# Kernel optimization log

Measured on AMD Instinct MI355X. Metric: run time of the kernel, lower is better.

Reference implementation:

```python
import jax, jax.numpy as jnp
import numpy as np

H = 12
D_MODEL = 768
D_K = D_MODEL // H  # 64


def setup_inputs() -> dict:
    key = jax.random.key(0)
    ks = jax.random.split(key, 16)
    B, S, D = 4, 1024, D_MODEL
    scale = 1.0 / np.sqrt(D)
    inp = {
        "query": jax.random.normal(ks[0], (B, S, D), jnp.float32),
        "key": jax.random.normal(ks[1], (B, S, D), jnp.float32),
        "value": jax.random.normal(ks[2], (B, S, D), jnp.float32),
        "times": jax.random.normal(ks[3], (2, B, S, D), jnp.float32),
        # learned params (Linear weights stored torch-style [out, in])
        "Wq": jax.random.normal(ks[4], (D, D), jnp.float32) * scale,
        "bq": jnp.zeros((D,), jnp.float32),
        "Wk": jax.random.normal(ks[5], (D, D), jnp.float32) * scale,
        "bk": jnp.zeros((D,), jnp.float32),
        "Wv": jax.random.normal(ks[6], (D, D), jnp.float32) * scale,
        "bv": jnp.zeros((D,), jnp.float32),
        "Wt": jax.random.normal(ks[7], (D, D), jnp.float32) * scale,
        "bt": jnp.zeros((D,), jnp.float32),
        "Wo": jax.random.normal(ks[8], (D, D), jnp.float32) * scale,
        "bo": jnp.zeros((D,), jnp.float32),
    }
    return inp


def _split_heads(x, B, S):
    # [B,S,D] -> [B,H,S,D_K]
    return x.reshape(B, S, H, D_K).transpose(0, 2, 1, 3)


def reference(query, key, value, times, Wq, bq, Wk, bk, Wv, bv, Wt, bt, Wo, bo):
    B, S, D = query.shape
    inv_sqrt_dk = 1.0 / jnp.sqrt(jnp.asarray(D_K, query.dtype))
    # q/k/v projections are identical across time-loop iterations; hoist them.
    q = _split_heads(query @ Wq.T + bq, B, S)   # [B,H,S,dk]
    k = _split_heads(key @ Wk.T + bk, B, S)
    v = _split_heads(value @ Wv.T + bv, B, S)
    x = jnp.zeros_like(q)
    n_times = times.shape[0]
    for i in range(n_times):  # small fixed loop over time embeddings
        t = _split_heads(times[i] @ Wt.T + bt, B, S)
        # dual-score attention: query.time + query.key, each scaled by 1/sqrt(d_k)
        scores = (jnp.einsum('bhqd,bhkd->bhqk', q, t)
                  + jnp.einsum('bhqd,bhkd->bhqk', q, k)) * inv_sqrt_dk
        p = jax.nn.softmax(scores, axis=-1)
        x = x + jnp.einsum('bhqk,bhkd->bhqd', p, v)
    x = x.transpose(0, 2, 1, 3).reshape(B, S, H * D_K)
    return x @ Wo.T + bo
```

## Files before the change

kernel.cpp:

```cpp
#include <hip/hip_runtime.h>
#include <hip/hip_fp16.h>

typedef _Float16 v8h __attribute__((ext_vector_type(8)));
typedef _Float16 v4h __attribute__((ext_vector_type(4)));
typedef float v4f __attribute__((ext_vector_type(4)));

#define MFMA_F16 __builtin_amdgcn_mfma_f32_16x16x32_f16
#define MFMA16_F16 __builtin_amdgcn_mfma_f32_16x16x16f16
#define EXP2F __builtin_amdgcn_exp2f

__device__ static inline void async_copy16(const void* g, void* l) {
  __builtin_amdgcn_global_load_lds(
      (const __attribute__((address_space(1))) void*)g,
      (__attribute__((address_space(3))) void*)l, 16, 0, 0);
}

struct CastArgs {
  const float* src[10];
  _Float16* dst[10];
  int n8[10];
  float scale[10];
};
__global__ void cast_all(CastArgs a) {
  const int z = blockIdx.y;
  const int i = blockIdx.x * 256 + threadIdx.x;
  if (i >= a.n8[z]) return;
  const float sc = a.scale[z];
  const float* s = a.src[z] + (size_t)i * 8;
  const float4 f0 = *(const float4*)s;
  const float4 f1 = *(const float4*)(s + 4);
  v8h o = {(_Float16)(f0.x * sc), (_Float16)(f0.y * sc),
           (_Float16)(f0.z * sc), (_Float16)(f0.w * sc),
           (_Float16)(f1.x * sc), (_Float16)(f1.y * sc),
           (_Float16)(f1.z * sc), (_Float16)(f1.w * sc)};
  *(v8h*)(a.dst[z] + (size_t)i * 8) = o;
}

struct GemmArgs {
  const _Float16* A1[4]; const _Float16* A2[4];
  const _Float16* W1[4]; const _Float16* W2[4];
  const float* b1[4];    const float* b2[4];
  void* out[4];
  float bscale[4];
  int K[4];
  int mode[4];
};

__global__ __launch_bounds__(256) void gemm_mt(GemmArgs g) {
  __shared__ _Float16 a_lds[128 * 64];
  __shared__ _Float16 w_lds[128 * 64];
  const int z = blockIdx.z;
  const int KK = g.K[z];
  const int tid = threadIdx.x;
  const int w = tid >> 6, lane = tid & 63, quad = lane >> 4, l16 = lane & 15;
  const int m0 = blockIdx.x * 128, n0 = blockIdx.y * 128;
  const int wm = (w >> 1) * 64, wn = (w & 1) * 64;

  size_t srcOff[4]; int ldsOff[4];
  #pragma unroll
  for (int i = 0; i < 4; ++i) {
    const int c = i * 256 + tid, row = c >> 3, slot = c & 7;
    srcOff[i] = (size_t)row * 768 + (size_t)((slot ^ (row & 7)) * 8);
    ldsOff[i] = (i * 256 + w * 64) * 8;
  }

  v4f acc[4][4] = {};

  for (int k0 = 0; k0 < KK; k0 += 64) {
    const _Float16* Asrc = (k0 < 768) ? g.A1[z] : g.A2[z];
    const _Float16* Wsrc = (k0 < 768) ? g.W1[z] : g.W2[z];
    const int kc = (k0 < 768) ? k0 : k0 - 768;
    __syncthreads();
    #pragma unroll
    for (int i = 0; i < 4; ++i) {
      async_copy16(Asrc + (size_t)m0 * 768 + kc + srcOff[i], &a_lds[ldsOff[i]]);
      async_copy16(Wsrc + (size_t)n0 * 768 + kc + srcOff[i], &w_lds[ldsOff[i]]);
    }
    __syncthreads();

    #pragma unroll
    for (int kh = 0; kh < 2; ++kh) {
      v8h af[4], bf[4];
      #pragma unroll
      for (int mt = 0; mt < 4; ++mt) {
        const int r = wm + mt * 16 + l16;
        af[mt] = *(const v8h*)&a_lds[r * 64 + (((kh * 4 + quad) ^ (r & 7)) * 8)];
      }
      #pragma unroll
      for (int nt = 0; nt < 4; ++nt) {
        const int r = wn + nt * 16 + l16;
        bf[nt] = *(const v8h*)&w_lds[r * 64 + (((kh * 4 + quad) ^ (r & 7)) * 8)];
      }
      #pragma unroll
      for (int mt = 0; mt < 4; ++mt)
        #pragma unroll
        for (int nt = 0; nt < 4; ++nt)
          acc[mt][nt] = MFMA_F16(af[mt], bf[nt], acc[mt][nt], 0, 0, 0);
    }
  }

  const int mode = g.mode[z];
  #pragma unroll
  for (int nt = 0; nt < 4; ++nt) {
    const int col = n0 + wn + nt * 16 + l16;
    float bv = g.b1[z][col] * g.bscale[z];
    if (g.b2[z]) bv += g.b2[z][col];
    if (mode == 1) {
      _Float16* outp = (_Float16*)g.out[z];
      const int h = col >> 6, dk = col & 63;
      #pragma unroll
      for (int mt = 0; mt < 4; ++mt) {
        const int row = m0 + wm + mt * 16 + quad * 4;
        const int b = row >> 10, s = row & 1023;
        const int sp = (s & ~31) | ((s & 12) << 1) | ((s & 16) >> 2);
        v4h pack = {(_Float16)(acc[mt][nt][0] + bv), (_Float16)(acc[mt][nt][1] + bv),
                    (_Float16)(acc[mt][nt][2] + bv), (_Float16)(acc[mt][nt][3] + bv)};
        *(v4h*)&outp[(size_t)((b * 12 + h) * 64 + dk) * 1024 + sp] = pack;
      }
    } else {
      #pragma unroll
      for (int mt = 0; mt < 4; ++mt)
        #pragma unroll
        for (int r = 0; r < 4; ++r) {
          const int row = m0 + wm + mt * 16 + quad * 4 + r;
          const float v = acc[mt][nt][r] + bv;
          if (mode == 2) ((float*)g.out[z])[(size_t)row * 768 + col] = v;
          else ((_Float16*)g.out[z])[(size_t)row * 768 + col] = (_Float16)v;
        }
    }
  }
}

__global__ __launch_bounds__(256) void attn(
    const _Float16* __restrict__ Q,
    const _Float16* __restrict__ KT0, const _Float16* __restrict__ KT1,
    const _Float16* __restrict__ Vt,
    _Float16* __restrict__ X)
{
  __shared__ _Float16 kt0[2][64 * 64];
  __shared__ _Float16 kt1[2][64 * 64];
  __shared__ _Float16 vt[2][64 * 64];

  const int tid = threadIdx.x;
  const int w = tid >> 6, lane = tid & 63, quad = lane >> 4, l16 = lane & 15;
  const int bh = blockIdx.y, b = bh / 12, h = bh % 12;
  const int q0 = blockIdx.x * 64;
  const size_t base = (size_t)b * 1024 * 768 + h * 64;

  const _Float16* KT0b = KT0 + base;
  const _Float16* KT1b = KT1 + base;
  const _Float16* Vtb = Vt + (size_t)bh * 64 * 1024;

  size_t ktOff[2], vOff[2]; int ldsOff[2];
  #pragma unroll
  for (int i = 0; i < 2; ++i) {
    const int c = i * 256 + w * 64 + lane, row = c >> 3, slot = c & 7;
    const int logical = slot ^ (row & 7);
    ktOff[i] = (size_t)row * 768 + (size_t)(logical * 8);
    vOff[i] = (size_t)row * 1024 + (size_t)(logical * 8);
    ldsOff[i] = c * 8;
  }
  auto stage = [&](int kv0, int buf) {
    #pragma unroll
    for (int i = 0; i < 2; ++i) {
      async_copy16(KT0b + (size_t)kv0 * 768 + ktOff[i], &kt0[buf][ldsOff[i]]);
      async_copy16(KT1b + (size_t)kv0 * 768 + ktOff[i], &kt1[buf][ldsOff[i]]);
      async_copy16(Vtb + (size_t)kv0 + vOff[i], &vt[buf][ldsOff[i]]);
    }
  };

  const _Float16* Qw = Q + base + (size_t)(q0 + w * 16) * 768;
  const v8h qf0 = *(const v8h*)(Qw + (size_t)l16 * 768 + quad * 8);
  const v8h qf1 = *(const v8h*)(Qw + (size_t)l16 * 768 + 32 + quad * 8);

  const v4h ones = {(_Float16)1.f, (_Float16)1.f, (_Float16)1.f, (_Float16)1.f};
  v4f o[2][4] = {};
  v4f osum[2] = {};

  stage(0, 0);
  for (int cc = 0; cc < 16; ++cc) {
    __syncthreads();
    if (cc < 15) stage((cc + 1) * 64, (cc + 1) & 1);
    const _Float16* k0p = &kt0[cc & 1][0];
    const _Float16* k1p = &kt1[cc & 1][0];
    const _Float16* vp = &vt[cc & 1][0];

    v4f s[2][4];
    #pragma unroll
    for (int kvt = 0; kvt < 4; ++kvt) {
      const int r = kvt * 16 + l16, rw = r & 7;
      const v8h k00 = *(const v8h*)&k0p[r * 64 + ((quad ^ rw) * 8)];
      const v8h k01 = *(const v8h*)&k0p[r * 64 + (((4 + quad) ^ rw) * 8)];
      const v8h k10 = *(const v8h*)&k1p[r * 64 + ((quad ^ rw) * 8)];
      const v8h k11 = *(const v8h*)&k1p[r * 64 + (((4 + quad) ^ rw) * 8)];
      s[0][kvt] = MFMA_F16(k00, qf0, v4f{}, 0, 0, 0);
      s[0][kvt] = MFMA_F16(k01, qf1, s[0][kvt], 0, 0, 0);
      s[1][kvt] = MFMA_F16(k10, qf0, v4f{}, 0, 0, 0);
      s[1][kvt] = MFMA_F16(k11, qf1, s[1][kvt], 0, 0, 0);
    }

    v4h pb[2][4];
    #pragma unroll
    for (int t = 0; t < 2; ++t)
      #pragma unroll
      for (int kvt = 0; kvt < 4; ++kvt) {
        pb[t][kvt] = v4h{(_Float16)EXP2F(s[t][kvt][0]),
                         (_Float16)EXP2F(s[t][kvt][1]),
                         (_Float16)EXP2F(s[t][kvt][2]),
                         (_Float16)EXP2F(s[t][kvt][3])};
        osum[t] = MFMA16_F16(ones, pb[t][kvt], osum[t], 0, 0, 0);
      }

    #pragma unroll
    for (int dkt = 0; dkt < 4; ++dkt) {
      const int row = dkt * 16 + l16, rw = row & 7;
      #pragma unroll
      for (int gph = 0; gph < 2; ++gph) {
        const int phys = (gph * 4 + quad) ^ rw;
        const v8h vv = *(const v8h*)&vp[row * 64 + phys * 8];
        const v4h lo = {vv[0], vv[1], vv[2], vv[3]};
        const v4h hi = {vv[4], vv[5], vv[6], vv[7]};
        #pragma unroll
        for (int t = 0; t < 2; ++t) {
          o[t][dkt] = MFMA16_F16(lo, pb[t][gph * 2], o[t][dkt], 0, 0, 0);
          o[t][dkt] = MFMA16_F16(hi, pb[t][gph * 2 + 1], o[t][dkt], 0, 0, 0);
        }
      }
    }
  }

  const float i0 = 1.0f / osum[0][0], i1 = 1.0f / osum[1][0];

  _Float16* Xw = X + base + (size_t)(q0 + w * 16 + l16) * 768;
  #pragma unroll
  for (int dkt = 0; dkt < 4; ++dkt) {
    v4h pack;
    #pragma unroll
    for (int r = 0; r < 4; ++r)
      pack[r] = (_Float16)(o[0][dkt][r] * i0 + o[1][dkt][r] * i1);
    *(v4h*)&Xw[dkt * 16 + quad * 4] = pack;
  }
}

extern "C" void kernel_launch(void* const* d_in, const int* in_sizes, int n_in,
                              void* d_out, int out_size, void* d_ws, size_t ws_size,
                              hipStream_t stream) {
  const float* query = (const float*)d_in[0];
  const float* key   = (const float*)d_in[1];
  const float* value = (const float*)d_in[2];
  const float* times = (const float*)d_in[3];
  const float* Wq = (const float*)d_in[4];  const float* bq = (const float*)d_in[5];
  const float* Wk = (const float*)d_in[6];  const float* bk = (const float*)d_in[7];
  const float* Wv = (const float*)d_in[8];  const float* bv = (const float*)d_in[9];
  const float* Wt = (const float*)d_in[10]; const float* bt = (const float*)d_in[11];
  const float* Wo = (const float*)d_in[12]; const float* bo = (const float*)d_in[13];
  float* out = (float*)d_out;

  const size_t NELEM = (size_t)4096 * 768;
  const size_t WELEM = (size_t)768 * 768;
  const float QSCALE = 0.125f * 1.4426950408889634f;

  char* ws = (char*)d_ws;
  size_t off = 0;
  auto alloc = [&](size_t bytes) {
    void* p = ws + off; off += (bytes + 255) & ~(size_t)255; return p;
  };
  _Float16* qh  = (_Float16*)alloc(NELEM * 2);
  _Float16* kh  = (_Float16*)alloc(NELEM * 2);
  _Float16* vh  = (_Float16*)alloc(NELEM * 2);
  _Float16* wqh = (_Float16*)alloc(WELEM * 2);
  _Float16* wkh = (_Float16*)alloc(WELEM * 2);
  _Float16* wvh = (_Float16*)alloc(WELEM * 2);
  _Float16* wth = (_Float16*)alloc(WELEM * 2);
  _Float16* woh = (_Float16*)alloc(WELEM * 2);
  _Float16* Qh  = (_Float16*)alloc(NELEM * 2);
  _Float16* KT0 = (_Float16*)alloc(NELEM * 2);
  _Float16* KT1 = (_Float16*)alloc(NELEM * 2);
  _Float16* Vt  = (_Float16*)alloc(NELEM * 2);
  _Float16* t0h = (_Float16*)d_out;
  _Float16* t1h = t0h + NELEM;
  _Float16* Xh = qh;

  CastArgs ca = {};
  const int nA8 = (int)(NELEM / 8), nW8 = (int)(WELEM / 8);
  const float* csrc[10] = {query, key, value, times, times + NELEM, Wq, Wk, Wv, Wt, Wo};
  _Float16* cdst[10] = {qh, kh, vh, t0h, t1h, wqh, wkh, wvh, wth, woh};
  for (int i = 0; i < 10; ++i) {
    ca.src[i] = csrc[i]; ca.dst[i] = cdst[i];
    ca.n8[i] = (i < 5) ? nA8 : nW8;
    ca.scale[i] = (i == 5) ? QSCALE : 1.0f;
  }
  cast_all<<<dim3((nA8 + 255) / 256, 10), 256, 0, stream>>>(ca);

  GemmArgs pa = {};
  pa.A1[0] = t0h; pa.A2[0] = kh; pa.W1[0] = wth; pa.W2[0] = wkh;
  pa.b1[0] = bt; pa.b2[0] = bk; pa.out[0] = KT0; pa.bscale[0] = 1.0f;
  pa.K[0] = 1536; pa.mode[0] = 0;
  pa.A1[1] = t1h; pa.A2[1] = kh; pa.W1[1] = wth; pa.W2[1] = wkh;
  pa.b1[1] = bt; pa.b2[1] = bk; pa.out[1] = KT1; pa.bscale[1] = 1.0f;
  pa.K[1] = 1536; pa.mode[1] = 0;
  pa.A1[2] = qh; pa.A2[2] = qh; pa.W1[2] = wqh; pa.W2[2] = wqh;
  pa.b1[2] = bq; pa.b2[2] = nullptr; pa.out[2] = Qh; pa.bscale[2] = QSCALE;
  pa.K[2] = 768; pa.mode[2] = 0;
  pa.A1[3] = vh; pa.A2[3] = vh; pa.W1[3] = wvh; pa.W2[3] = wvh;
  pa.b1[3] = bv; pa.b2[3] = nullptr; pa.out[3] = Vt; pa.bscale[3] = 1.0f;
  pa.K[3] = 768; pa.mode[3] = 1;
  gemm_mt<<<dim3(32, 6, 4), 256, 0, stream>>>(pa);

  attn<<<dim3(16, 48), 256, 0, stream>>>(Qh, KT0, KT1, Vt, Xh);

  GemmArgs oa = {};
  oa.A1[0] = Xh; oa.A2[0] = Xh; oa.W1[0] = woh; oa.W2[0] = woh;
  oa.b1[0] = bo; oa.b2[0] = nullptr; oa.out[0] = out; oa.bscale[0] = 1.0f;
  oa.K[0] = 768; oa.mode[0] = 2;
  gemm_mt<<<dim3(32, 6, 1), 256, 0, stream>>>(oa);
}
```

Baseline: 237.8 us.

## Use 16x16x32 MFMA for PV, flatten cast grid, smaller output-GEMM tiles

The attention PV and row-sum products switch from the 16x16x16 MFMA to the 16x16x32 MFMA. P is packed with cvt_pkrtz into 8-wide fp16 vectors so each V LDS read feeds a single MFMA. The main loop is unrolled by two so LDS buffer pointers become constants. The cast kernel moves from a 2D grid with idle blocks for the small weight tensors to a flat 1D grid with prefix offsets. The output projection GEMM uses a templated 64-row tile so it launches twice as many blocks. These changes cut instruction count, wasted blocks and output-GEMM underfill, at the cost of round-toward-zero fp16 conversion of the probabilities.

```diff
diff --git a/kernel.cpp b/kernel.cpp
--- a/kernel.cpp
+++ b/kernel.cpp
@@ -3,11 +3,15 @@
 
 typedef _Float16 v8h __attribute__((ext_vector_type(8)));
 typedef _Float16 v4h __attribute__((ext_vector_type(4)));
+typedef _Float16 v2h __attribute__((ext_vector_type(2)));
 typedef float v4f __attribute__((ext_vector_type(4)));
 
 #define MFMA_F16 __builtin_amdgcn_mfma_f32_16x16x32_f16
-#define MFMA16_F16 __builtin_amdgcn_mfma_f32_16x16x16f16
 #define EXP2F __builtin_amdgcn_exp2f
+
+__device__ static inline v2h pkrtz(float a, float b) {
+  return __builtin_bit_cast(v2h, __builtin_amdgcn_cvt_pkrtz(a, b));
+}
 
 __device__ static inline void async_copy16(const void* g, void* l) {
   __builtin_amdgcn_global_load_lds(
@@ -18,22 +22,25 @@
 struct CastArgs {
   const float* src[10];
   _Float16* dst[10];
-  int n8[10];
+  int start[11];
   float scale[10];
 };
 __global__ void cast_all(CastArgs a) {
-  const int z = blockIdx.y;
-  const int i = blockIdx.x * 256 + threadIdx.x;
-  if (i >= a.n8[z]) return;
+  const int g = blockIdx.x * 256 + threadIdx.x;
+  if (g >= a.start[10]) return;
+  int z = 0;
+  #pragma unroll
+  for (int i = 1; i < 10; ++i) if (g >= a.start[i]) z = i;
+  const int i0 = g - a.start[z];
   const float sc = a.scale[z];
-  const float* s = a.src[z] + (size_t)i * 8;
+  const float* s = a.src[z] + (size_t)i0 * 8;
   const float4 f0 = *(const float4*)s;
   const float4 f1 = *(const float4*)(s + 4);
   v8h o = {(_Float16)(f0.x * sc), (_Float16)(f0.y * sc),
            (_Float16)(f0.z * sc), (_Float16)(f0.w * sc),
            (_Float16)(f1.x * sc), (_Float16)(f1.y * sc),
            (_Float16)(f1.z * sc), (_Float16)(f1.w * sc)};
-  *(v8h*)(a.dst[z] + (size_t)i * 8) = o;
+  *(v8h*)(a.dst[z] + (size_t)i0 * 8) = o;
 }
 
 struct GemmArgs {
@@ -46,15 +53,18 @@
   int mode[4];
 };
 
+template <int MT>
 __global__ __launch_bounds__(256) void gemm_mt(GemmArgs g) {
-  __shared__ _Float16 a_lds[128 * 64];
+  constexpr int iA = MT / 32;
+  constexpr int NMT = MT / 32;
+  __shared__ _Float16 a_lds[MT * 64];
   __shared__ _Float16 w_lds[128 * 64];
   const int z = blockIdx.z;
   const int KK = g.K[z];
   const int tid = threadIdx.x;
   const int w = tid >> 6, lane = tid & 63, quad = lane >> 4, l16 = lane & 15;
-  const int m0 = blockIdx.x * 128, n0 = blockIdx.y * 128;
-  const int wm = (w >> 1) * 64, wn = (w & 1) * 64;
+  const int m0 = blockIdx.x * MT, n0 = blockIdx.y * 128;
+  const int wm = (w >> 1) * (MT / 2), wn = (w & 1) * 64;
 
   size_t srcOff[4]; int ldsOff[4];
   #pragma unroll
@@ -64,7 +74,7 @@
     ldsOff[i] = (i * 256 + w * 64) * 8;
   }
 
-  v4f acc[4][4] = {};
+  v4f acc[NMT][4] = {};
 
   for (int k0 = 0; k0 < KK; k0 += 64) {
     const _Float16* Asrc = (k0 < 768) ? g.A1[z] : g.A2[z];
@@ -73,16 +83,17 @@
     __syncthreads();
     #pragma unroll
     for (int i = 0; i < 4; ++i) {
-      async_copy16(Asrc + (size_t)m0 * 768 + kc + srcOff[i], &a_lds[ldsOff[i]]);
+      if (i < iA)
+        async_copy16(Asrc + (size_t)m0 * 768 + kc + srcOff[i], &a_lds[ldsOff[i]]);
       async_copy16(Wsrc + (size_t)n0 * 768 + kc + srcOff[i], &w_lds[ldsOff[i]]);
     }
     __syncthreads();
 
     #pragma unroll
     for (int kh = 0; kh < 2; ++kh) {
-      v8h af[4], bf[4];
-      #pragma unroll
-      for (int mt = 0; mt < 4; ++mt) {
+      v8h af[NMT], bf[4];
+      #pragma unroll
+      for (int mt = 0; mt < NMT; ++mt) {
         const int r = wm + mt * 16 + l16;
         af[mt] = *(const v8h*)&a_lds[r * 64 + (((kh * 4 + quad) ^ (r & 7)) * 8)];
       }
@@ -92,7 +103,7 @@
         bf[nt] = *(const v8h*)&w_lds[r * 64 + (((kh * 4 + quad) ^ (r & 7)) * 8)];
       }
       #pragma unroll
-      for (int mt = 0; mt < 4; ++mt)
+      for (int mt = 0; mt < NMT; ++mt)
         #pragma unroll
         for (int nt = 0; nt < 4; ++nt)
           acc[mt][nt] = MFMA_F16(af[mt], bf[nt], acc[mt][nt], 0, 0, 0);
@@ -109,7 +120,7 @@
       _Float16* outp = (_Float16*)g.out[z];
       const int h = col >> 6, dk = col & 63;
       #pragma unroll
-      for (int mt = 0; mt < 4; ++mt) {
+      for (int mt = 0; mt < NMT; ++mt) {
         const int row = m0 + wm + mt * 16 + quad * 4;
         const int b = row >> 10, s = row & 1023;
         const int sp = (s & ~31) | ((s & 12) << 1) | ((s & 16) >> 2);
@@ -119,7 +130,7 @@
       }
     } else {
       #pragma unroll
-      for (int mt = 0; mt < 4; ++mt)
+      for (int mt = 0; mt < NMT; ++mt)
         #pragma unroll
         for (int r = 0; r < 4; ++r) {
           const int row = m0 + wm + mt * 16 + quad * 4 + r;
@@ -173,17 +184,15 @@
   const v8h qf0 = *(const v8h*)(Qw + (size_t)l16 * 768 + quad * 8);
   const v8h qf1 = *(const v8h*)(Qw + (size_t)l16 * 768 + 32 + quad * 8);
 
-  const v4h ones = {(_Float16)1.f, (_Float16)1.f, (_Float16)1.f, (_Float16)1.f};
+  const _Float16 one = (_Float16)1.f;
+  const v8h ones8 = {one, one, one, one, one, one, one, one};
   v4f o[2][4] = {};
   v4f osum[2] = {};
 
-  stage(0, 0);
-  for (int cc = 0; cc < 16; ++cc) {
+  auto body = [&](int cc, const _Float16* k0p, const _Float16* k1p,
+                  const _Float16* vp) {
     __syncthreads();
     if (cc < 15) stage((cc + 1) * 64, (cc + 1) & 1);
-    const _Float16* k0p = &kt0[cc & 1][0];
-    const _Float16* k1p = &kt1[cc & 1][0];
-    const _Float16* vp = &vt[cc & 1][0];
 
     v4f s[2][4];
     #pragma unroll
@@ -199,34 +208,37 @@
       s[1][kvt] = MFMA_F16(k11, qf1, s[1][kvt], 0, 0, 0);
     }
 
-    v4h pb[2][4];
+    v8h pb8[2][2];
     #pragma unroll
     for (int t = 0; t < 2; ++t)
       #pragma unroll
-      for (int kvt = 0; kvt < 4; ++kvt) {
-        pb[t][kvt] = v4h{(_Float16)EXP2F(s[t][kvt][0]),
-                         (_Float16)EXP2F(s[t][kvt][1]),
-                         (_Float16)EXP2F(s[t][kvt][2]),
-                         (_Float16)EXP2F(s[t][kvt][3])};
-        osum[t] = MFMA16_F16(ones, pb[t][kvt], osum[t], 0, 0, 0);
+      for (int gg = 0; gg < 2; ++gg) {
+        const v4f sa = s[t][gg * 2], sb = s[t][gg * 2 + 1];
+        const v2h a0 = pkrtz(EXP2F(sa[0]), EXP2F(sa[1]));
+        const v2h a1 = pkrtz(EXP2F(sa[2]), EXP2F(sa[3]));
+        const v2h b0 = pkrtz(EXP2F(sb[0]), EXP2F(sb[1]));
+        const v2h b1 = pkrtz(EXP2F(sb[2]), EXP2F(sb[3]));
+        pb8[t][gg] = v8h{a0[0], a0[1], a1[0], a1[1], b0[0], b0[1], b1[0], b1[1]};
+        osum[t] = MFMA_F16(ones8, pb8[t][gg], osum[t], 0, 0, 0);
       }
 
     #pragma unroll
     for (int dkt = 0; dkt < 4; ++dkt) {
       const int row = dkt * 16 + l16, rw = row & 7;
       #pragma unroll
-      for (int gph = 0; gph < 2; ++gph) {
-        const int phys = (gph * 4 + quad) ^ rw;
-        const v8h vv = *(const v8h*)&vp[row * 64 + phys * 8];
-        const v4h lo = {vv[0], vv[1], vv[2], vv[3]};
-        const v4h hi = {vv[4], vv[5], vv[6], vv[7]};
-        #pragma unroll
-        for (int t = 0; t < 2; ++t) {
-          o[t][dkt] = MFMA16_F16(lo, pb[t][gph * 2], o[t][dkt], 0, 0, 0);
-          o[t][dkt] = MFMA16_F16(hi, pb[t][gph * 2 + 1], o[t][dkt], 0, 0, 0);
-        }
-      }
-    }
+      for (int gg = 0; gg < 2; ++gg) {
+        const int slot = (gg * 4 + quad) ^ rw;
+        const v8h vv = *(const v8h*)&vp[row * 64 + slot * 8];
+        o[0][dkt] = MFMA_F16(vv, pb8[0][gg], o[0][dkt], 0, 0, 0);
+        o[1][dkt] = MFMA_F16(vv, pb8[1][gg], o[1][dkt], 0, 0, 0);
+      }
+    }
+  };
+
+  stage(0, 0);
+  for (int it = 0; it < 8; ++it) {
+    body(it * 2, &kt0[0][0], &kt1[0][0], &vt[0][0]);
+    body(it * 2 + 1, &kt0[1][0], &kt1[1][0], &vt[1][0]);
   }
 
   const float i0 = 1.0f / osum[0][0], i1 = 1.0f / osum[1][0];
@@ -285,12 +297,15 @@
   const int nA8 = (int)(NELEM / 8), nW8 = (int)(WELEM / 8);
   const float* csrc[10] = {query, key, value, times, times + NELEM, Wq, Wk, Wv, Wt, Wo};
   _Float16* cdst[10] = {qh, kh, vh, t0h, t1h, wqh, wkh, wvh, wth, woh};
+  int acc8 = 0;
   for (int i = 0; i < 10; ++i) {
     ca.src[i] = csrc[i]; ca.dst[i] = cdst[i];
-    ca.n8[i] = (i < 5) ? nA8 : nW8;
+    ca.start[i] = acc8;
+    acc8 += (i < 5) ? nA8 : nW8;
     ca.scale[i] = (i == 5) ? QSCALE : 1.0f;
   }
-  cast_all<<<dim3((nA8 + 255) / 256, 10), 256, 0, stream>>>(ca);
+  ca.start[10] = acc8;
+  cast_all<<<dim3((acc8 + 255) / 256), 256, 0, stream>>>(ca);
 
   GemmArgs pa = {};
   pa.A1[0] = t0h; pa.A2[0] = kh; pa.W1[0] = wth; pa.W2[0] = wkh;
@@ -305,7 +320,7 @@
   pa.A1[3] = vh; pa.A2[3] = vh; pa.W1[3] = wvh; pa.W2[3] = wvh;
   pa.b1[3] = bv; pa.b2[3] = nullptr; pa.out[3] = Vt; pa.bscale[3] = 1.0f;
   pa.K[3] = 768; pa.mode[3] = 1;
-  gemm_mt<<<dim3(32, 6, 4), 256, 0, stream>>>(pa);
+  gemm_mt<128><<<dim3(32, 6, 4), 256, 0, stream>>>(pa);
 
   attn<<<dim3(16, 48), 256, 0, stream>>>(Qh, KT0, KT1, Vt, Xh);
 
@@ -313,5 +328,5 @@
   oa.A1[0] = Xh; oa.A2[0] = Xh; oa.W1[0] = woh; oa.W2[0] = woh;
   oa.b1[0] = bo; oa.b2[0] = nullptr; oa.out[0] = out; oa.bscale[0] = 1.0f;
   oa.K[0] = 768; oa.mode[0] = 2;
-  gemm_mt<<<dim3(32, 6, 1), 256, 0, stream>>>(oa);
-}
+  gemm_mt<64><<<dim3(64, 6, 1), 256, 0, stream>>>(oa);
+}
```

Measured after the change: 229.9 us. -3.3%, faster.
